# Optimization experiments

Measured on AMD Instinct MI355X. Metric: run time of the kernel, lower is better.

The kernel has to match this reference:

```python
import jax, jax.numpy as jnp
import numpy as np
import math

EMB_DIM = 1024
HEAD_SIZE = 64
T = 4096
B = 4

def setup_inputs() -> dict:
    key = jax.random.key(0)
    k1, k2, k3, k4 = jax.random.split(key, 4)
    scale = 1.0 / math.sqrt(EMB_DIM)
    return {
        "input": jax.random.normal(k1, (B, T, EMB_DIM), dtype=jnp.float32),
        "Wq": jax.random.normal(k2, (EMB_DIM, HEAD_SIZE), dtype=jnp.float32) * scale,
        "Wk": jax.random.normal(k3, (EMB_DIM, HEAD_SIZE), dtype=jnp.float32) * scale,
        "Wv": jax.random.normal(k4, (EMB_DIM, HEAD_SIZE), dtype=jnp.float32) * scale,
    }

def reference(input, Wq, Wk, Wv):
    # q,k,v: [B,T,H]
    q = input @ Wq
    k = input @ Wk
    v = input @ Wv
    # scores: [B,T,T]
    match = jnp.einsum('bqh,bkh->bqk', q, k)
    # 'encoder' mask in this repo = causal tril mask
    causal = jnp.tril(jnp.ones((T, T), dtype=bool))
    match = jnp.where(causal, match, -jnp.inf)
    # NOTE: faithful to source quirk: softmax first, THEN divide by sqrt(head_size)
    attention = jax.nn.softmax(match, axis=-1) / math.sqrt(HEAD_SIZE)
    return jnp.einsum('bqk,bkh->bqh', attention, v)
```

## Files before the change

kernel.cpp:

```cpp
#include <hip/hip_runtime.h>

#define T_SEQ 4096
#define NBATCH 4
#define EMB 1024
#define HS 64
#define BT (NBATCH * T_SEQ)

typedef float f32x4 __attribute__((ext_vector_type(4)));
typedef short s16x8 __attribute__((ext_vector_type(8)));

__device__ __forceinline__ unsigned short f2bf(float x) {
  union { float f; unsigned u; } c; c.f = x;
  unsigned r = c.u + 0x7FFF + ((c.u >> 16) & 1);
  return (unsigned short)(r >> 16);
}
__device__ __forceinline__ float bf2f(unsigned short h) {
  union { unsigned u; float f; } c; c.u = ((unsigned)h) << 16;
  return c.f;
}
__device__ __forceinline__ void cvt8(float4 a0, float4 a1, s16x8& hi, s16x8& lo) {
  float xv[8] = {a0.x, a0.y, a0.z, a0.w, a1.x, a1.y, a1.z, a1.w};
#pragma unroll
  for (int j = 0; j < 8; ++j) {
    unsigned short h = f2bf(xv[j]);
    hi[j] = (short)h;
    lo[j] = (short)f2bf(xv[j] - bf2f(h));
  }
}
__device__ __forceinline__ void cvt8t(float4 a0, float4 a1, s16x8& hi, s16x8& lo) {
  float xv[8] = {a0.x, a0.y, a0.z, a0.w, a1.x, a1.y, a1.z, a1.w};
  unsigned hu[8], lu[8];
#pragma unroll
  for (int j = 0; j < 8; ++j) {
    union { float f; unsigned u; } c; c.f = xv[j];
    hu[j] = c.u;
    union { unsigned u; float f; } hf; hf.u = c.u & 0xFFFF0000u;
    union { float f; unsigned u; } r; r.f = xv[j] - hf.f;
    lu[j] = r.u;
  }
  union { s16x8 v; unsigned u[4]; } H, L;
#pragma unroll
  for (int j = 0; j < 4; ++j) {
    H.u[j] = (hu[2 * j] >> 16) | (hu[2 * j + 1] & 0xFFFF0000u);
    L.u[j] = (lu[2 * j] >> 16) | (lu[2 * j + 1] & 0xFFFF0000u);
  }
  hi = H.v; lo = L.v;
}

__global__ __launch_bounds__(256) void wconv(
    const float* __restrict__ Wq, const float* __restrict__ Wk,
    const float* __restrict__ Wv, unsigned short* __restrict__ wt_hi,
    unsigned short* __restrict__ wt_lo) {
  const int n3 = blockIdx.x;
  const int which = n3 >> 6, n = n3 & 63;
  const float* W = (which == 0) ? Wq : (which == 1) ? Wk : Wv;
#pragma unroll
  for (int i = 0; i < 4; ++i) {
    int k = i * 256 + threadIdx.x;
    float x = W[(size_t)k * HS + n];
    unsigned short h = f2bf(x);
    wt_hi[(size_t)n3 * EMB + k] = h;
    wt_lo[(size_t)n3 * EMB + k] = f2bf(x - bf2f(h));
  }
}

__global__ __launch_bounds__(512) void qkv_mfma(
    const float* __restrict__ inp, const unsigned short* __restrict__ wt_hi,
    const unsigned short* __restrict__ wt_lo, float* __restrict__ qf,
    unsigned short* __restrict__ khi, unsigned short* __restrict__ klo,
    unsigned short* __restrict__ vtb) {
  __shared__ unsigned short Bh0[192 * 72];
  __shared__ unsigned short Bl0[192 * 72];
  __shared__ unsigned short Bh1[192 * 72];
  __shared__ unsigned short Bl1[192 * 72];
  const int t = threadIdx.x, lane = t & 63, w = t >> 6;
  const int m = lane & 15, quad = lane >> 4;
  const int mg = w >> 1, ng = w & 1;
  const int tok0 = blockIdx.x * 64;
  const int arow = tok0 + mg * 16 + m;

  f32x4 acc[6];
#pragma unroll
  for (int nt = 0; nt < 6; ++nt) acc[nt] = (f32x4){0.f, 0.f, 0.f, 0.f};

  const int s0 = t, s1 = t + 512, s2 = t + 1024;
  const int n3_0 = s0 >> 3, k8_0 = s0 & 7;
  const int n3_1 = s1 >> 3, k8_1 = s1 & 7;
  const int n3_2 = s2 >> 3, k8_2 = s2 & 7;
  const size_t goff0 = (size_t)n3_0 * EMB + k8_0 * 8;
  const size_t goff1 = (size_t)n3_1 * EMB + k8_1 * 8;
  const size_t goff2 = (size_t)n3_2 * EMB + k8_2 * 8;
  const int lds0 = n3_0 * 72 + k8_0 * 8;
  const int lds1 = n3_1 * 72 + k8_1 * 8;
  const int lds2 = n3_2 * 72 + k8_2 * 8;

#define LOAD_B(K0, PH0, PH1, PH2, PL0, PL1, PL2)            \
  PH0 = *(const uint4*)&wt_hi[goff0 + (K0)];                \
  PH1 = *(const uint4*)&wt_hi[goff1 + (K0)];                \
  PH2 = *(const uint4*)&wt_hi[goff2 + (K0)];                \
  PL0 = *(const uint4*)&wt_lo[goff0 + (K0)];                \
  PL1 = *(const uint4*)&wt_lo[goff1 + (K0)];                \
  PL2 = *(const uint4*)&wt_lo[goff2 + (K0)];

#define STORE_B(BH, BL, PH0, PH1, PH2, PL0, PL1, PL2)       \
  *(uint4*)&BH[lds0] = PH0;                                 \
  *(uint4*)&BH[lds1] = PH1;                                 \
  *(uint4*)&BH[lds2] = PH2;                                 \
  *(uint4*)&BL[lds0] = PL0;                                 \
  *(uint4*)&BL[lds1] = PL1;                                 \
  *(uint4*)&BL[lds2] = PL2;

#define LOAD_A(K0, PA0, PA1, PA2, PA3)                      \
  {                                                         \
    const float* ap = &inp[(size_t)arow * EMB + (K0) + quad * 8]; \
    PA0 = *(const float4*)ap;                               \
    PA1 = *(const float4*)(ap + 4);                         \
    PA2 = *(const float4*)(ap + 32);                        \
    PA3 = *(const float4*)(ap + 36);                        \
  }

#define QKV_TILE(BH, BL, AH0, AL0, AH1, AL1)                                 \
  {                                                                          \
    _Pragma("unroll")                                                        \
    for (int nt = 0; nt < 6; ++nt) {                                         \
      const int bbase = (ng * 96 + nt * 16 + m) * 72;                        \
      f32x4 a = acc[nt];                                                     \
      {                                                                      \
        s16x8 bh = *(const s16x8*)&BH[bbase + quad * 8];                     \
        s16x8 bl = *(const s16x8*)&BL[bbase + quad * 8];                     \
        a = __builtin_amdgcn_mfma_f32_16x16x32_bf16(AH0, bh, a, 0, 0, 0);    \
        a = __builtin_amdgcn_mfma_f32_16x16x32_bf16(AH0, bl, a, 0, 0, 0);    \
        a = __builtin_amdgcn_mfma_f32_16x16x32_bf16(AL0, bh, a, 0, 0, 0);    \
      }                                                                      \
      {                                                                      \
        s16x8 bh = *(const s16x8*)&BH[bbase + 32 + quad * 8];                \
        s16x8 bl = *(const s16x8*)&BL[bbase + 32 + quad * 8];                \
        a = __builtin_amdgcn_mfma_f32_16x16x32_bf16(AH1, bh, a, 0, 0, 0);    \
        a = __builtin_amdgcn_mfma_f32_16x16x32_bf16(AH1, bl, a, 0, 0, 0);    \
        a = __builtin_amdgcn_mfma_f32_16x16x32_bf16(AL1, bh, a, 0, 0, 0);    \
      }                                                                      \
      acc[nt] = a;                                                           \
    }                                                                        \
  }

  uint4 phA0, phA1, phA2, plA0, plA1, plA2;
  uint4 phB0, phB1, phB2, plB0, plB1, plB2;
  float4 paA0, paA1, paA2, paA3;
  float4 paB0, paB1, paB2, paB3;

  LOAD_B(0, phA0, phA1, phA2, plA0, plA1, plA2);
  LOAD_A(0, paA0, paA1, paA2, paA3);
  STORE_B(Bh0, Bl0, phA0, phA1, phA2, plA0, plA1, plA2);
  LOAD_B(64, phB0, phB1, phB2, plB0, plB1, plB2);
  LOAD_A(64, paB0, paB1, paB2, paB3);
  __syncthreads();

#pragma unroll 1
  for (int kc = 0; kc < 8; ++kc) {
    const int kbase = kc * 128;
    STORE_B(Bh1, Bl1, phB0, phB1, phB2, plB0, plB1, plB2);
    if (kc < 7) { LOAD_B(kbase + 128, phA0, phA1, phA2, plA0, plA1, plA2); }
    {
      s16x8 ah0, al0, ah1, al1;
      cvt8t(paA0, paA1, ah0, al0);
      cvt8t(paA2, paA3, ah1, al1);
      if (kc < 7) { LOAD_A(kbase + 128, paA0, paA1, paA2, paA3); }
      QKV_TILE(Bh0, Bl0, ah0, al0, ah1, al1);
    }
    __syncthreads();
    if (kc < 7) { STORE_B(Bh0, Bl0, phA0, phA1, phA2, plA0, plA1, plA2); }
    {
      s16x8 ah0, al0, ah1, al1;
      cvt8t(paB0, paB1, ah0, al0);
      cvt8t(paB2, paB3, ah1, al1);
      if (kc < 7) {
        LOAD_B(kbase + 192, phB0, phB1, phB2, plB0, plB1, plB2);
        LOAD_A(kbase + 192, paB0, paB1, paB2, paB3);
      }
      QKV_TILE(Bh1, Bl1, ah0, al0, ah1, al1);
    }
    if (kc < 7) __syncthreads();
  }

#undef LOAD_B
#undef STORE_B
#undef LOAD_A
#undef QKV_TILE

#pragma unroll
  for (int nt = 0; nt < 6; ++nt) {
    int n3 = ng * 96 + nt * 16 + m;
    int which = n3 >> 6, col = n3 & 63;
#pragma unroll
    for (int r = 0; r < 4; ++r) {
      int tok = tok0 + mg * 16 + quad * 4 + r;
      float val = acc[nt][r];
      if (which == 0) {
        qf[(size_t)tok * HS + col] = val;
      } else if (which == 1) {
        unsigned short h = f2bf(val);
        khi[(size_t)tok * HS + col] = h;
        klo[(size_t)tok * HS + col] = f2bf(val - bf2f(h));
      } else {
        vtb[(size_t)(tok >> 6) * 4096 + (size_t)col * 64 + (tok & 63)] = f2bf(val);
      }
    }
  }
}

__global__ __launch_bounds__(256) void attn_part(
    const float* __restrict__ q, const unsigned short* __restrict__ khi,
    const unsigned short* __restrict__ klo, const unsigned short* __restrict__ vt,
    unsigned short* __restrict__ partO, float* __restrict__ partML) {
  __shared__ unsigned short Khi_s[64 * 72];
  __shared__ unsigned short Klo_s[64 * 72];
  __shared__ unsigned short Vt_s[64 * 72];
  __shared__ unsigned short P_s[4 * 16 * 72];
  const int t = threadIdx.x;
  const int lane = t & 63, w = t >> 6;
  const int m = lane & 15, quad = lane >> 4;

  int u = blockIdx.x;
  const int b = u / 160;
  u -= b * 160;
  int qtile = 0, c = 0;
  {
    int acc2 = 0;
    for (int qq = 0; qq < 64; ++qq) {
      int ncq = (qq >> 4) + 1;
      if (u < acc2 + ncq) { qtile = qq; c = u - acc2; break; }
      acc2 += ncq;
    }
  }
  const int kt0 = c * 16;
  const int kt1 = (kt0 + 16 < qtile + 1) ? kt0 + 16 : qtile + 1;

  const size_t qrow0 = (size_t)b * T_SEQ + (size_t)qtile * 64;
  const size_t krowbase = (size_t)b * T_SEQ;
  const int q_loc = w * 16 + m;

  s16x8 qh[2], ql[2];
#pragma unroll
  for (int cc = 0; cc < 2; ++cc) {
    const float* qp = &q[(qrow0 + q_loc) * HS + cc * 32 + quad * 8];
    cvt8(*(const float4*)qp, *(const float4*)(qp + 4), qh[cc], ql[cc]);
  }

  float l_st = 0.f;
  f32x4 o[4];
#pragma unroll
  for (int hb = 0; hb < 4; ++hb) o[hb] = (f32x4){0.f, 0.f, 0.f, 0.f};

  const int r0 = t >> 3, ch0 = t & 7;
  const int r1 = (256 + t) >> 3, ch1 = t & 7;

  uint4 pk0h, pk0l, pv0, pk1h, pk1l, pv1;
  {
    size_t g0 = (krowbase + (size_t)kt0 * 64 + r0) * HS + ch0 * 8;
    size_t g1 = (krowbase + (size_t)kt0 * 64 + r1) * HS + ch1 * 8;
    pk0h = *(const uint4*)&khi[g0]; pk0l = *(const uint4*)&klo[g0];
    pk1h = *(const uint4*)&khi[g1]; pk1l = *(const uint4*)&klo[g1];
    size_t v0 = (size_t)(b * 64 + kt0) * 4096 + (size_t)r0 * 64 + ch0 * 8;
    size_t v1 = (size_t)(b * 64 + kt0) * 4096 + (size_t)r1 * 64 + ch1 * 8;
    pv0 = *(const uint4*)&vt[v0]; pv1 = *(const uint4*)&vt[v1];
  }

  for (int kt = kt0; kt < kt1; ++kt) {
    __syncthreads();
    *(uint4*)&Khi_s[r0 * 72 + ch0 * 8] = pk0h;
    *(uint4*)&Klo_s[r0 * 72 + ch0 * 8] = pk0l;
    *(uint4*)&Vt_s[r0 * 72 + ch0 * 8] = pv0;
    *(uint4*)&Khi_s[r1 * 72 + ch1 * 8] = pk1h;
    *(uint4*)&Klo_s[r1 * 72 + ch1 * 8] = pk1l;
    *(uint4*)&Vt_s[r1 * 72 + ch1 * 8] = pv1;
    __syncthreads();

    if (kt + 1 < kt1) {
      size_t g0 = (krowbase + (size_t)(kt + 1) * 64 + r0) * HS + ch0 * 8;
      size_t g1 = (krowbase + (size_t)(kt + 1) * 64 + r1) * HS + ch1 * 8;
      pk0h = *(const uint4*)&khi[g0]; pk0l = *(const uint4*)&klo[g0];
      pk1h = *(const uint4*)&khi[g1]; pk1l = *(const uint4*)&klo[g1];
      size_t v0 = (size_t)(b * 64 + kt + 1) * 4096 + (size_t)r0 * 64 + ch0 * 8;
      size_t v1 = (size_t)(b * 64 + kt + 1) * 4096 + (size_t)r1 * 64 + ch1 * 8;
      pv0 = *(const uint4*)&vt[v0]; pv1 = *(const uint4*)&vt[v1];
    }

    f32x4 st[4];
#pragma unroll
    for (int cb = 0; cb < 4; ++cb) {
      st[cb] = (f32x4){0.f, 0.f, 0.f, 0.f};
#pragma unroll
      for (int cc = 0; cc < 2; ++cc) {
        s16x8 bh = *(const s16x8*)&Khi_s[(cb * 16 + m) * 72 + cc * 32 + quad * 8];
        s16x8 bl = *(const s16x8*)&Klo_s[(cb * 16 + m) * 72 + cc * 32 + quad * 8];
        st[cb] = __builtin_amdgcn_mfma_f32_16x16x32_bf16(bh, qh[cc], st[cb], 0, 0, 0);
        st[cb] = __builtin_amdgcn_mfma_f32_16x16x32_bf16(bl, qh[cc], st[cb], 0, 0, 0);
        st[cb] = __builtin_amdgcn_mfma_f32_16x16x32_bf16(bh, ql[cc], st[cb], 0, 0, 0);
      }
    }
    if (kt == qtile) {
#pragma unroll
      for (int cb = 0; cb < 4; ++cb)
#pragma unroll
        for (int r = 0; r < 4; ++r)
          if (cb * 16 + quad * 4 + r > q_loc) st[cb][r] = -1e30f;
    }
#pragma unroll
    for (int cb = 0; cb < 4; ++cb)
#pragma unroll
      for (int r = 0; r < 4; ++r) {
        st[cb][r] = __expf(st[cb][r]);
        l_st += st[cb][r];
      }
#pragma unroll
    for (int cb = 0; cb < 4; ++cb) {
      uint2 pk;
      pk.x = (unsigned)f2bf(st[cb][0]) | ((unsigned)f2bf(st[cb][1]) << 16);
      pk.y = (unsigned)f2bf(st[cb][2]) | ((unsigned)f2bf(st[cb][3]) << 16);
      *(uint2*)&P_s[q_loc * 72 + cb * 16 + quad * 4] = pk;
    }
    s16x8 pf[2];
#pragma unroll
    for (int cc = 0; cc < 2; ++cc)
      pf[cc] = *(const s16x8*)&P_s[q_loc * 72 + cc * 32 + quad * 8];
#pragma unroll
    for (int hb = 0; hb < 4; ++hb) {
#pragma unroll
      for (int cc = 0; cc < 2; ++cc) {
        s16x8 vf = *(const s16x8*)&Vt_s[(hb * 16 + m) * 72 + cc * 32 + quad * 8];
        o[hb] = __builtin_amdgcn_mfma_f32_16x16x32_bf16(vf, pf[cc], o[hb], 0, 0, 0);
      }
    }
  }

  l_st += __shfl_xor(l_st, 16, 64);
  l_st += __shfl_xor(l_st, 32, 64);

  const int slot = ((b * 64 + qtile) << 2) + c;
  unsigned short* Op = partO + (size_t)slot * 4096;
#pragma unroll
  for (int hb = 0; hb < 4; ++hb) {
    uint2 pk;
    pk.x = (unsigned)f2bf(o[hb][0]) | ((unsigned)f2bf(o[hb][1]) << 16);
    pk.y = (unsigned)f2bf(o[hb][2]) | ((unsigned)f2bf(o[hb][3]) << 16);
    *(uint2*)&Op[q_loc * 64 + hb * 16 + quad * 4] = pk;
  }
  if (quad == 0) partML[(size_t)slot * 64 + q_loc] = l_st;
}

__global__ __launch_bounds__(256) void attn_combine(
    const unsigned short* __restrict__ partO, const float* __restrict__ partML,
    float* __restrict__ out) {
  const int qtile = blockIdx.x, b = blockIdx.y;
  const int t = threadIdx.x;
  const int row = t >> 2, hg = t & 3;
  const int nc = (qtile >> 4) + 1;
  const int slot0 = (b * 64 + qtile) << 2;

  float lsum = 0.f;
  for (int i = 0; i < nc; ++i) lsum += partML[(size_t)(slot0 + i) * 64 + row];
  const float inv = 1.f / (lsum * 8.0f);

  float acc[16];
#pragma unroll
  for (int e = 0; e < 16; ++e) acc[e] = 0.f;
  for (int i = 0; i < nc; ++i) {
    const unsigned short* Op =
        partO + (size_t)(slot0 + i) * 4096 + row * 64 + hg * 16;
    uint4 u0 = *(const uint4*)Op;
    uint4 u1 = *(const uint4*)(Op + 8);
    unsigned uv[8] = {u0.x, u0.y, u0.z, u0.w, u1.x, u1.y, u1.z, u1.w};
#pragma unroll
    for (int e = 0; e < 8; ++e) {
      acc[2 * e] += bf2f((unsigned short)(uv[e] & 0xFFFF));
      acc[2 * e + 1] += bf2f((unsigned short)(uv[e] >> 16));
    }
  }
  float* op = &out[((size_t)b * T_SEQ + (size_t)qtile * 64 + row) * HS + hg * 16];
#pragma unroll
  for (int v = 0; v < 4; ++v) {
    float4 r;
    r.x = acc[4 * v + 0] * inv; r.y = acc[4 * v + 1] * inv;
    r.z = acc[4 * v + 2] * inv; r.w = acc[4 * v + 3] * inv;
    ((float4*)op)[v] = r;
  }
}

extern "C" void kernel_launch(void* const* d_in, const int* in_sizes, int n_in,
                              void* d_out, int out_size, void* d_ws, size_t ws_size,
                              hipStream_t stream) {
  const float* inp = (const float*)d_in[0];
  const float* Wq  = (const float*)d_in[1];
  const float* Wk  = (const float*)d_in[2];
  const float* Wv  = (const float*)d_in[3];
  float* out = (float*)d_out;

  char* base = (char*)d_ws;
  float* qf = (float*)base;
  unsigned short* khi = (unsigned short*)(base + (size_t)BT * HS * 4);
  unsigned short* klo = khi + (size_t)BT * HS;
  unsigned short* vtb = klo + (size_t)BT * HS;
  unsigned short* wt_hi = vtb + (size_t)BT * HS;
  unsigned short* wt_lo = wt_hi + (size_t)192 * EMB;
  unsigned short* partO = wt_lo + (size_t)192 * EMB;
  float* partML = (float*)(partO + (size_t)1024 * 4096);

  wconv<<<dim3(192), dim3(256), 0, stream>>>(Wq, Wk, Wv, wt_hi, wt_lo);
  qkv_mfma<<<dim3(BT / 64), dim3(512), 0, stream>>>(inp, wt_hi, wt_lo, qf, khi, klo, vtb);
  attn_part<<<dim3(640), dim3(256), 0, stream>>>(qf, khi, klo, vtb, partO, partML);
  attn_combine<<<dim3(64, NBATCH), dim3(256), 0, stream>>>(partO, partML, out);
}
```

Measured before the change: 168.5 us.

## Stage QKV weight tiles via direct global-to-LDS loads with XOR swizzle

Replaces the register-staged weight loads (global to VGPR, then LDS store) in the QKV projection kernel with global_load_lds 16-byte direct transfers into double-buffered shared memory. The padded 72-stride layout becomes an XOR-swizzled 64-stride layout to avoid bank conflicts. This cuts VGPR pressure and ds_write instructions, at the cost of relying on the sync placement being correct for the asynchronous LDS fills. It only affects the QKV stage, not the attention kernel that likely dominates the runtime.

```diff
diff --git a/kernel.cpp b/kernel.cpp
--- a/kernel.cpp
+++ b/kernel.cpp
@@ -45,6 +45,12 @@
     L.u[j] = (lu[2 * j] >> 16) | (lu[2 * j + 1] & 0xFFFF0000u);
   }
   hi = H.v; lo = L.v;
+}
+
+__device__ __forceinline__ void gl16(const void* g, void* l) {
+  __builtin_amdgcn_global_load_lds(
+      (const __attribute__((address_space(1))) void*)g,
+      (__attribute__((address_space(3))) void*)l, 16, 0, 0);
 }
 
 __global__ __launch_bounds__(256) void wconv(
@@ -69,10 +75,8 @@
     const unsigned short* __restrict__ wt_lo, float* __restrict__ qf,
     unsigned short* __restrict__ khi, unsigned short* __restrict__ klo,
     unsigned short* __restrict__ vtb) {
-  __shared__ unsigned short Bh0[192 * 72];
-  __shared__ unsigned short Bl0[192 * 72];
-  __shared__ unsigned short Bh1[192 * 72];
-  __shared__ unsigned short Bl1[192 * 72];
+  __shared__ __align__(16) unsigned short S0[24576];
+  __shared__ __align__(16) unsigned short S1[24576];
   const int t = threadIdx.x, lane = t & 63, w = t >> 6;
   const int m = lane & 15, quad = lane >> 4;
   const int mg = w >> 1, ng = w & 1;
@@ -83,58 +87,47 @@
 #pragma unroll
   for (int nt = 0; nt < 6; ++nt) acc[nt] = (f32x4){0.f, 0.f, 0.f, 0.f};
 
-  const int s0 = t, s1 = t + 512, s2 = t + 1024;
-  const int n3_0 = s0 >> 3, k8_0 = s0 & 7;
-  const int n3_1 = s1 >> 3, k8_1 = s1 & 7;
-  const int n3_2 = s2 >> 3, k8_2 = s2 & 7;
-  const size_t goff0 = (size_t)n3_0 * EMB + k8_0 * 8;
-  const size_t goff1 = (size_t)n3_1 * EMB + k8_1 * 8;
-  const size_t goff2 = (size_t)n3_2 * EMB + k8_2 * 8;
-  const int lds0 = n3_0 * 72 + k8_0 * 8;
-  const int lds1 = n3_1 * 72 + k8_1 * 8;
-  const int lds2 = n3_2 * 72 + k8_2 * 8;
-
-#define LOAD_B(K0, PH0, PH1, PH2, PL0, PL1, PL2)            \
-  PH0 = *(const uint4*)&wt_hi[goff0 + (K0)];                \
-  PH1 = *(const uint4*)&wt_hi[goff1 + (K0)];                \
-  PH2 = *(const uint4*)&wt_hi[goff2 + (K0)];                \
-  PL0 = *(const uint4*)&wt_lo[goff0 + (K0)];                \
-  PL1 = *(const uint4*)&wt_lo[goff1 + (K0)];                \
-  PL2 = *(const uint4*)&wt_lo[goff2 + (K0)];
-
-#define STORE_B(BH, BL, PH0, PH1, PH2, PL0, PL1, PL2)       \
-  *(uint4*)&BH[lds0] = PH0;                                 \
-  *(uint4*)&BH[lds1] = PH1;                                 \
-  *(uint4*)&BH[lds2] = PH2;                                 \
-  *(uint4*)&BL[lds0] = PL0;                                 \
-  *(uint4*)&BL[lds1] = PL1;                                 \
-  *(uint4*)&BL[lds2] = PL2;
-
-#define LOAD_A(K0, PA0, PA1, PA2, PA3)                      \
-  {                                                         \
-    const float* ap = &inp[(size_t)arow * EMB + (K0) + quad * 8]; \
-    PA0 = *(const float4*)ap;                               \
-    PA1 = *(const float4*)(ap + 4);                         \
-    PA2 = *(const float4*)(ap + 32);                        \
-    PA3 = *(const float4*)(ap + 36);                        \
-  }
-
-#define QKV_TILE(BH, BL, AH0, AL0, AH1, AL1)                                 \
+  const int rl = lane >> 3;
+  const int cl = ((lane & 7) ^ rl) * 8;
+  const unsigned short* ghi = wt_hi + (size_t)(w * 8 + rl) * EMB + cl;
+  const unsigned short* glo = wt_lo + (size_t)(w * 8 + rl) * EMB + cl;
+  unsigned short* const l0 = S0 + w * 512;
+  unsigned short* const l1 = S1 + w * 512;
+
+#define STAGE(LB, K0)                                    \
+  gl16(ghi + (K0), (LB));                                \
+  gl16(ghi + 64 * EMB + (K0), (LB) + 4096);              \
+  gl16(ghi + 128 * EMB + (K0), (LB) + 8192);             \
+  gl16(glo + (K0), (LB) + 12288);                        \
+  gl16(glo + 64 * EMB + (K0), (LB) + 16384);             \
+  gl16(glo + 128 * EMB + (K0), (LB) + 20480);
+
+#define LOAD_A(K0, PA0, PA1, PA2, PA3)                               \
+  {                                                                  \
+    const float* ap = &inp[(size_t)arow * EMB + (K0) + quad * 8];    \
+    PA0 = *(const float4*)ap;        PA1 = *(const float4*)(ap + 4); \
+    PA2 = *(const float4*)(ap + 32); PA3 = *(const float4*)(ap + 36);\
+  }
+
+  const int csw0 = (quad ^ (m & 7)) * 8;
+  const int csw1 = ((quad + 4) ^ (m & 7)) * 8;
+
+#define QKV_TILE(S, AH0, AL0, AH1, AL1)                                      \
   {                                                                          \
     _Pragma("unroll")                                                        \
     for (int nt = 0; nt < 6; ++nt) {                                         \
-      const int bbase = (ng * 96 + nt * 16 + m) * 72;                        \
+      const int bb = (ng * 96 + nt * 16 + m) * 64;                           \
       f32x4 a = acc[nt];                                                     \
       {                                                                      \
-        s16x8 bh = *(const s16x8*)&BH[bbase + quad * 8];                     \
-        s16x8 bl = *(const s16x8*)&BL[bbase + quad * 8];                     \
+        s16x8 bh = *(const s16x8*)&S[bb + csw0];                             \
+        s16x8 bl = *(const s16x8*)&S[12288 + bb + csw0];                     \
         a = __builtin_amdgcn_mfma_f32_16x16x32_bf16(AH0, bh, a, 0, 0, 0);    \
         a = __builtin_amdgcn_mfma_f32_16x16x32_bf16(AH0, bl, a, 0, 0, 0);    \
         a = __builtin_amdgcn_mfma_f32_16x16x32_bf16(AL0, bh, a, 0, 0, 0);    \
       }                                                                      \
       {                                                                      \
-        s16x8 bh = *(const s16x8*)&BH[bbase + 32 + quad * 8];                \
-        s16x8 bl = *(const s16x8*)&BL[bbase + 32 + quad * 8];                \
+        s16x8 bh = *(const s16x8*)&S[bb + csw1];                             \
+        s16x8 bl = *(const s16x8*)&S[12288 + bb + csw1];                     \
         a = __builtin_amdgcn_mfma_f32_16x16x32_bf16(AH1, bh, a, 0, 0, 0);    \
         a = __builtin_amdgcn_mfma_f32_16x16x32_bf16(AH1, bl, a, 0, 0, 0);    \
         a = __builtin_amdgcn_mfma_f32_16x16x32_bf16(AL1, bh, a, 0, 0, 0);    \
@@ -143,47 +136,37 @@
     }                                                                        \
   }
 
-  uint4 phA0, phA1, phA2, plA0, plA1, plA2;
-  uint4 phB0, phB1, phB2, plB0, plB1, plB2;
   float4 paA0, paA1, paA2, paA3;
   float4 paB0, paB1, paB2, paB3;
 
-  LOAD_B(0, phA0, phA1, phA2, plA0, plA1, plA2);
+  STAGE(l0, 0);
   LOAD_A(0, paA0, paA1, paA2, paA3);
-  STORE_B(Bh0, Bl0, phA0, phA1, phA2, plA0, plA1, plA2);
-  LOAD_B(64, phB0, phB1, phB2, plB0, plB1, plB2);
   LOAD_A(64, paB0, paB1, paB2, paB3);
   __syncthreads();
 
 #pragma unroll 1
   for (int kc = 0; kc < 8; ++kc) {
-    const int kbase = kc * 128;
-    STORE_B(Bh1, Bl1, phB0, phB1, phB2, plB0, plB1, plB2);
-    if (kc < 7) { LOAD_B(kbase + 128, phA0, phA1, phA2, plA0, plA1, plA2); }
+    STAGE(l1, (2 * kc + 1) * 64);
     {
       s16x8 ah0, al0, ah1, al1;
       cvt8t(paA0, paA1, ah0, al0);
       cvt8t(paA2, paA3, ah1, al1);
-      if (kc < 7) { LOAD_A(kbase + 128, paA0, paA1, paA2, paA3); }
-      QKV_TILE(Bh0, Bl0, ah0, al0, ah1, al1);
+      if (kc < 7) { LOAD_A((2 * kc + 2) * 64, paA0, paA1, paA2, paA3); }
+      QKV_TILE(S0, ah0, al0, ah1, al1);
     }
     __syncthreads();
-    if (kc < 7) { STORE_B(Bh0, Bl0, phA0, phA1, phA2, plA0, plA1, plA2); }
+    if (kc < 7) { STAGE(l0, (2 * kc + 2) * 64); }
     {
       s16x8 ah0, al0, ah1, al1;
       cvt8t(paB0, paB1, ah0, al0);
       cvt8t(paB2, paB3, ah1, al1);
-      if (kc < 7) {
-        LOAD_B(kbase + 192, phB0, phB1, phB2, plB0, plB1, plB2);
-        LOAD_A(kbase + 192, paB0, paB1, paB2, paB3);
-      }
-      QKV_TILE(Bh1, Bl1, ah0, al0, ah1, al1);
+      if (kc < 7) { LOAD_A((2 * kc + 3) * 64, paB0, paB1, paB2, paB3); }
+      QKV_TILE(S1, ah0, al0, ah1, al1);
     }
     if (kc < 7) __syncthreads();
   }
 
-#undef LOAD_B
-#undef STORE_B
+#undef STAGE
 #undef LOAD_A
 #undef QKV_TILE
 
```

Result: slower. 172.5 us (+2.4%).
